# Performance work log

Measured on AMD Instinct MI355X. Metric: run time of the kernel, lower is better.

## Reference

```python
import jax, jax.numpy as jnp
import numpy as np

NUM_HEADS = 16
D_MODEL = 1024
SEQ = 4096
HEAD_DIM = D_MODEL // NUM_HEADS
ROPE_BASE = 10000.0


def _rope(x):
    # x: [h, s, d]  (rotate-half RoPE per head)
    s, d = x.shape[-2], x.shape[-1]
    inv_freq = 1.0 / (ROPE_BASE ** (jnp.arange(0, d, 2, dtype=jnp.float32) / d))  # [d/2]
    ang = jnp.arange(s, dtype=jnp.float32)[:, None] * inv_freq[None, :]           # [s, d/2]
    cos, sin = jnp.cos(ang), jnp.sin(ang)
    x1, x2 = x[..., : d // 2], x[..., d // 2 :]
    return jnp.concatenate([x1 * cos - x2 * sin, x1 * sin + x2 * cos], axis=-1)


def setup_inputs() -> dict:
    key = jax.random.key(0)
    kq, kk, kv, kwq, kwk, kwv = jax.random.split(key, 6)
    scale = 1.0 / np.sqrt(D_MODEL)
    return {
        "q": jax.random.normal(kq, (SEQ, D_MODEL), dtype=jnp.float32),
        "k": jax.random.normal(kk, (SEQ, D_MODEL), dtype=jnp.float32),
        "v": jax.random.normal(kv, (SEQ, D_MODEL), dtype=jnp.float32),
        "mask": jnp.tril(jnp.ones((SEQ, SEQ), dtype=bool)),  # causal
        "Wq": jax.random.normal(kwq, (D_MODEL, D_MODEL), dtype=jnp.float32) * scale,
        "Wk": jax.random.normal(kwk, (D_MODEL, D_MODEL), dtype=jnp.float32) * scale,
        "Wv": jax.random.normal(kwv, (D_MODEL, D_MODEL), dtype=jnp.float32) * scale,
    }


def reference(q, k, v, mask, Wq, Wk, Wv):
    # Projections (eqx Linear: x @ W.T, no bias)
    qp = q @ Wq.T  # [s, d_model]
    kp = k @ Wk.T
    vp = v @ Wv.T
    # split heads: [s, (h d)] -> [h, s, d]
    def split(x):
        return x.reshape(SEQ, NUM_HEADS, HEAD_DIM).transpose(1, 0, 2)
    qh, kh, vh = split(qp), split(kp), split(vp)
    qh = _rope(qh)
    kh = _rope(kh)
    # explicit full logits, masked softmax (matches original, no SDPA)
    logits = jnp.einsum("hqd,hkd->hqk", qh, kh) / jnp.sqrt(jnp.float32(HEAD_DIM))
    logits = jnp.where(mask[None, :, :], logits, -jnp.inf)
    attn = jax.nn.softmax(logits, axis=-1)  # [h, q, k]
    out = jnp.einsum("hqk,hkd->hqd", attn, vh)
    return out.transpose(1, 0, 2).reshape(SEQ, D_MODEL)
```

## Files before the change

### kernel.cpp

```cpp
#include <hip/hip_runtime.h>
#include <math.h>

#define SEQ 4096
#define DMODEL 1024
#define NHEADS 16
#define HDIM 64

typedef __bf16 v8bf __attribute__((ext_vector_type(8)));
typedef float f32x4 __attribute__((ext_vector_type(4)));
typedef float f32x16 __attribute__((ext_vector_type(16)));
typedef int i32x2 __attribute__((ext_vector_type(2)));
typedef int i32x4 __attribute__((ext_vector_type(4)));

#define NPART 4608
#define SCALE_Q 0.18033688011112042f

__device__ __forceinline__ unsigned short f2bf(float f) {
    union { float f; unsigned int u; } v; v.f = f;
    unsigned int u = v.u;
    return (unsigned short)((u + 0x7fffu + ((u >> 16) & 1u)) >> 16);
}

__device__ __forceinline__ int cvtpk(float lo, float hi) {
    int r;
    asm("v_cvt_pk_bf16_f32 %0, %1, %2" : "=v"(r) : "v"(lo), "v"(hi));
    return r;
}

__device__ __forceinline__ void gload16(const unsigned short* g, unsigned short* l) {
    __builtin_amdgcn_global_load_lds(
        (const __attribute__((address_space(1))) unsigned int*)g,
        (__attribute__((address_space(3))) unsigned int*)l, 16, 0, 0);
}

__global__ __launch_bounds__(256) void cast_kernel(
    const float* __restrict__ q, const float* __restrict__ k, const float* __restrict__ v,
    const float* __restrict__ wq, const float* __restrict__ wk, const float* __restrict__ wv,
    unsigned short* __restrict__ xq, unsigned short* __restrict__ xk,
    unsigned short* __restrict__ xv, unsigned short* __restrict__ wb)
{
    const size_t M4 = (size_t)4 << 20, M1 = (size_t)1 << 20;
    size_t i = ((size_t)blockIdx.x * 256 + threadIdx.x) * 8;
    const float* s; unsigned short* d; size_t off;
    if (i < M4)                 { s = q;  d = xq;          off = i; }
    else if (i < 2 * M4)        { s = k;  d = xk;          off = i - M4; }
    else if (i < 3 * M4)        { s = v;  d = xv;          off = i - 2 * M4; }
    else if (i < 3 * M4 + M1)   { s = wq; d = wb;          off = i - 3 * M4; }
    else if (i < 3 * M4 + 2*M1) { s = wk; d = wb + M1;     off = i - 3 * M4 - M1; }
    else                        { s = wv; d = wb + 2 * M1; off = i - 3 * M4 - 2 * M1; }
    float4 a = *reinterpret_cast<const float4*>(s + off);
    float4 b = *reinterpret_cast<const float4*>(s + off + 4);
    uint4 u;
    u.x = (unsigned)cvtpk(a.x, a.y); u.y = (unsigned)cvtpk(a.z, a.w);
    u.z = (unsigned)cvtpk(b.x, b.y); u.w = (unsigned)cvtpk(b.z, b.w);
    *reinterpret_cast<uint4*>(d + off) = u;
}

__global__ __launch_bounds__(256) void proj_rope_kernel(
    const unsigned short* __restrict__ Xq, const unsigned short* __restrict__ Xk,
    const unsigned short* __restrict__ Xv, const unsigned short* __restrict__ Wb,
    unsigned short* __restrict__ qh, unsigned short* __restrict__ kfr,
    unsigned short* __restrict__ vfr)
{
    const int tz = blockIdx.z;
    const unsigned short* __restrict__ X = (tz == 0) ? Xq : (tz == 1) ? Xk : Xv;
    const unsigned short* __restrict__ W = Wb + (size_t)tz * ((size_t)1 << 20);

    const int tid = threadIdx.x;
    const int lane = tid & 63;
    const int wid = tid >> 6;
    const int l15 = lane & 15;
    const int l4 = lane >> 4;
    const int wr = wid >> 1, wc = wid & 1;

    const int m0 = blockIdx.x * 128;
    const int n0 = blockIdx.y * 128;

    __shared__ __align__(16) unsigned short Ab[2][4096];
    __shared__ __align__(16) unsigned short Bb[2][4096];

    int grow[2], gcol[2];
    #pragma unroll
    for (int g = 0; g < 2; ++g) {
        int row = wid * 32 + g * 16 + (lane >> 2);
        grow[g] = row;
        gcol[g] = 8 * ((lane & 3) ^ ((row >> 1) & 3));
    }

    auto STAGE = [&](int b, int kt) {
        const int k0 = kt << 5;
        #pragma unroll
        for (int g = 0; g < 2; ++g) {
            gload16(X + (size_t)(m0 + grow[g]) * DMODEL + k0 + gcol[g],
                    &Ab[b][(wid * 2 + g) * 512]);
            gload16(W + (size_t)(n0 + grow[g]) * DMODEL + k0 + gcol[g],
                    &Bb[b][(wid * 2 + g) * 512]);
        }
    };

    f32x4 acc[4][4] = {};

    STAGE(0, 0);
    for (int kt = 0; kt < 32; ++kt) {
        __syncthreads();
        if (kt < 31) STAGE((kt + 1) & 1, kt + 1);

        const unsigned short* A = Ab[kt & 1];
        const unsigned short* B = Bb[kt & 1];

        v8bf af[4], bfr[4];
        #pragma unroll
        for (int mi = 0; mi < 4; ++mi) {
            int row = wr * 64 + mi * 16 + l15;
            int byte = row * 64 + ((l4 ^ ((row >> 1) & 3)) << 4);
            af[mi] = *reinterpret_cast<const v8bf*>(reinterpret_cast<const char*>(A) + byte);
        }
        #pragma unroll
        for (int ni = 0; ni < 4; ++ni) {
            int row = wc * 64 + ni * 16 + l15;
            int byte = row * 64 + ((l4 ^ ((row >> 1) & 3)) << 4);
            bfr[ni] = *reinterpret_cast<const v8bf*>(reinterpret_cast<const char*>(B) + byte);
        }
        #pragma unroll
        for (int mi = 0; mi < 4; ++mi)
            #pragma unroll
            for (int ni = 0; ni < 4; ++ni)
                acc[mi][ni] = __builtin_amdgcn_mfma_f32_16x16x32_bf16(af[mi], bfr[ni], acc[mi][ni], 0, 0, 0);
    }

    const int h = (n0 >> 6) + wc;
    const int mbase = m0 + wr * 64;
    const int T = blockIdx.x * 2 + wr;

    if (tz == 2) {
        unsigned short* vb = vfr + (size_t)h * 262144 + (size_t)T * 4096;
        #pragma unroll
        for (int mi = 0; mi < 4; ++mi) {
            #pragma unroll
            for (int ni = 0; ni < 4; ++ni) {
                int f = (ni >> 1) * 4 + mi;
                int off = f * 512 + ((l4 >> 1) * 32 + (ni & 1) * 16 + l15) * 8 + (l4 & 1) * 4;
                uint2 pk;
                pk.x = (unsigned)cvtpk(acc[mi][ni][0], acc[mi][ni][1]);
                pk.y = (unsigned)cvtpk(acc[mi][ni][2], acc[mi][ni][3]);
                *reinterpret_cast<uint2*>(vb + off) = pk;
            }
        }
    } else if (tz == 1) {
        unsigned short* kb = kfr + (size_t)h * 262144 + (size_t)T * 4096;
        #pragma unroll
        for (int ni = 0; ni < 2; ++ni) {
            int j = ni * 16 + l15;
            float invf = expf(-(float)j * 0.28782313662425574f);
            #pragma unroll
            for (int mi = 0; mi < 4; ++mi) {
                #pragma unroll
                for (int r = 0; r < 4; ++r) {
                    int m = mbase + mi * 16 + l4 * 4 + r;
                    float ang = (float)m * invf;
                    float sn, cs;
                    sincosf(ang, &sn, &cs);
                    float x1 = acc[mi][ni][r];
                    float x2 = acc[mi][ni + 2][r];
                    int rowoff = ((l15 >> 3) * 32 + (mi & 1) * 16 + l4 * 4 + r) * 8 + (l15 & 7);
                    int fb = (mi >> 1) * 4;
                    kb[(fb + ni) * 512 + rowoff]     = f2bf(x1 * cs - x2 * sn);
                    kb[(fb + ni + 2) * 512 + rowoff] = f2bf(x1 * sn + x2 * cs);
                }
            }
        }
    } else {
        unsigned short* base = qh + (size_t)h * SEQ * HDIM;
        #pragma unroll
        for (int ni = 0; ni < 2; ++ni) {
            int j = ni * 16 + l15;
            float invf = expf(-(float)j * 0.28782313662425574f);
            #pragma unroll
            for (int mi = 0; mi < 4; ++mi) {
                #pragma unroll
                for (int r = 0; r < 4; ++r) {
                    int m = mbase + mi * 16 + l4 * 4 + r;
                    float ang = (float)m * invf;
                    float sn, cs;
                    sincosf(ang, &sn, &cs);
                    sn *= SCALE_Q; cs *= SCALE_Q;
                    float x1 = acc[mi][ni][r];
                    float x2 = acc[mi][ni + 2][r];
                    base[(size_t)m * HDIM + j]      = f2bf(x1 * cs - x2 * sn);
                    base[(size_t)m * HDIM + j + 32] = f2bf(x1 * sn + x2 * cs);
                }
            }
        }
    }
}

__global__ __launch_bounds__(64, 2) void attn_kernel(
    const unsigned short* __restrict__ qh, const unsigned short* __restrict__ kfr,
    const unsigned short* __restrict__ vfr, float* __restrict__ out,
    unsigned short* __restrict__ po, float* __restrict__ ml)
{
    const int lane = threadIdx.x & 63;
    const int l31 = lane & 31;
    const int l5 = lane >> 5;

    const int bid = blockIdx.x;
    const int xcd = bid & 7;
    const int idx = bid >> 3;
    const int hsel = (idx >= 320) ? 1 : 0;
    const int h = (xcd << 1) | hsel;
    const int r = 319 - (idx - hsel * 320);

    int qb, c, nc;
    if (r < 32)       { qb = r;                     c = 0;            nc = 1; }
    else if (r < 96)  { qb = 32 + ((r - 32) >> 1);  c = (r - 32) & 1; nc = 2; }
    else if (r < 192) { int rr = r - 96; qb = 64 + rr / 3; c = rr - (qb - 64) * 3; nc = 3; }
    else              { int rr = r - 192; qb = 96 + (rr >> 2); c = rr & 3; nc = 4; }

    const int q0 = qb * 32;
    const int q = q0 + l31;
    const int nt = (q0 + 32 + 63) >> 6;
    const int t0 = c * 16;
    const int t1 = min(t0 + 16, nt);

    const unsigned short* __restrict__ qbase = qh + ((size_t)h * SEQ + q) * HDIM + l5 * 8;
    const unsigned short* __restrict__ kfh = kfr + (size_t)h * 262144 + lane * 8;
    const unsigned short* __restrict__ vfh = vfr + (size_t)h * 262144 + lane * 8;

    v8bf qf[4];
    #pragma unroll
    for (int dk = 0; dk < 4; ++dk)
        qf[dk] = *reinterpret_cast<const v8bf*>(qbase + dk * 16);

    f32x16 of[2] = {};
    float mreg = -INFINITY, lreg = 0.0f;

    auto LOADK = [&](v8bf (&KB)[8], int T) {
        const unsigned short* kp = kfh + (size_t)T * 4096;
        #pragma unroll
        for (int f = 0; f < 8; ++f)
            KB[f] = *reinterpret_cast<const v8bf*>(kp + f * 512);
    };

    auto ROUND = [&](int T, v8bf (&KC)[8], v8bf (&KN)[8]) {
        v8bf vf[8];
        {
            const unsigned short* vp = vfh + (size_t)T * 4096;
            #pragma unroll
            for (int f = 0; f < 8; ++f)
                vf[f] = *reinterpret_cast<const v8bf*>(vp + f * 512);
        }
        if (T + 1 < t1) LOADK(KN, T + 1);

        f32x16 st[2];
        __builtin_amdgcn_s_setprio(1);
        #pragma unroll
        for (int ns = 0; ns < 2; ++ns) {
            f32x16 acc = {};
            #pragma unroll
            for (int dk = 0; dk < 4; ++dk)
                acc = __builtin_amdgcn_mfma_f32_32x32x16_bf16(KC[ns * 4 + dk], qf[dk], acc, 0, 0, 0);
            st[ns] = acc;
        }
        __builtin_amdgcn_s_setprio(0);

        if (T == nt - 1) {
            const int kvb = T * 64 + 4 * l5;
            #pragma unroll
            for (int ns = 0; ns < 2; ++ns)
                #pragma unroll
                for (int i = 0; i < 16; ++i) {
                    int kv = kvb + ns * 32 + (i & 3) + 8 * (i >> 2);
                    if (kv > q) st[ns][i] = -INFINITY;
                }
        }

        float t16[16];
        #pragma unroll
        for (int i = 0; i < 16; ++i) t16[i] = fmaxf(st[0][i], st[1][i]);
        #pragma unroll
        for (int i = 0; i < 8; ++i) t16[i] = fmaxf(t16[i], t16[i + 8]);
        #pragma unroll
        for (int i = 0; i < 4; ++i) t16[i] = fmaxf(t16[i], t16[i + 4]);
        float pmax = fmaxf(fmaxf(t16[0], t16[1]), fmaxf(t16[2], t16[3]));
        {
            i32x2 sw = __builtin_amdgcn_permlane32_swap(__float_as_int(pmax), __float_as_int(pmax), false, false);
            pmax = fmaxf(__int_as_float(sw.x), __int_as_float(sw.y));
        }

        if (!__all(pmax - mreg <= 8.0f)) {
            float mnew = fmaxf(mreg, pmax);
            float sc = exp2f(mreg - mnew);
            lreg *= sc;
            #pragma unroll
            for (int dt = 0; dt < 2; ++dt)
                #pragma unroll
                for (int i = 0; i < 16; ++i) of[dt][i] *= sc;
            mreg = mnew;
        }

        float ps0 = 0.f, ps1 = 0.f, ps2 = 0.f, ps3 = 0.f;
        #pragma unroll
        for (int ns = 0; ns < 2; ++ns)
            #pragma unroll
            for (int i = 0; i < 16; ++i) {
                float p = exp2f(st[ns][i] - mreg);
                st[ns][i] = p;
                if ((i & 3) == 0) ps0 += p; else if ((i & 3) == 1) ps1 += p;
                else if ((i & 3) == 2) ps2 += p; else ps3 += p;
            }
        lreg += (ps0 + ps1) + (ps2 + ps3);

        v8bf pt[4];
        #pragma unroll
        for (int kb = 0; kb < 4; ++kb) {
            int ns = kb >> 1, kp = (kb & 1) * 8;
            int A0 = cvtpk(st[ns][kp + 0], st[ns][kp + 1]);
            int A1 = cvtpk(st[ns][kp + 2], st[ns][kp + 3]);
            int B0 = cvtpk(st[ns][kp + 4], st[ns][kp + 5]);
            int B1 = cvtpk(st[ns][kp + 6], st[ns][kp + 7]);
            i32x2 s0 = __builtin_amdgcn_permlane32_swap(A0, B0, false, false);
            i32x2 s1 = __builtin_amdgcn_permlane32_swap(A1, B1, false, false);
            i32x4 u; u.x = s0.x; u.y = s1.x; u.z = s0.y; u.w = s1.y;
            v8bf p; __builtin_memcpy(&p, &u, 16);
            pt[kb] = p;
        }

        __builtin_amdgcn_s_setprio(1);
        #pragma unroll
        for (int dt = 0; dt < 2; ++dt)
            #pragma unroll
            for (int kb = 0; kb < 4; ++kb)
                of[dt] = __builtin_amdgcn_mfma_f32_32x32x16_bf16(vf[dt * 4 + kb], pt[kb], of[dt], 0, 0, 0);
        __builtin_amdgcn_s_setprio(0);
    };

    v8bf kA[8], kB[8];
    LOADK(kA, t0);
    int t = t0;
    while (true) {
        ROUND(t, kA, kB);
        if (++t == t1) break;
        ROUND(t, kB, kA);
        if (++t == t1) break;
    }

    {
        i32x2 sw = __builtin_amdgcn_permlane32_swap(__float_as_int(lreg), __float_as_int(lreg), false, false);
        lreg = __int_as_float(sw.x) + __int_as_float(sw.y);
    }

    if (nc == 1) {
        float inv = 1.0f / lreg;
        float* obase = out + (size_t)q * DMODEL + h * HDIM + l5 * 4;
        #pragma unroll
        for (int dt = 0; dt < 2; ++dt)
            #pragma unroll
            for (int g = 0; g < 4; ++g) {
                f32x4 o4;
                o4[0] = of[dt][g * 4 + 0] * inv;
                o4[1] = of[dt][g * 4 + 1] * inv;
                o4[2] = of[dt][g * 4 + 2] * inv;
                o4[3] = of[dt][g * 4 + 3] * inv;
                *reinterpret_cast<f32x4*>(obase + dt * 32 + g * 8) = o4;
            }
    } else {
        const int p = h * 288 + (r - 32);
        unsigned short* pb = po + ((size_t)p * 32 + l31) * 64 + l5 * 4;
        #pragma unroll
        for (int dt = 0; dt < 2; ++dt)
            #pragma unroll
            for (int g = 0; g < 4; ++g) {
                uint2 u;
                u.x = (unsigned)cvtpk(of[dt][g * 4 + 0], of[dt][g * 4 + 1]);
                u.y = (unsigned)cvtpk(of[dt][g * 4 + 2], of[dt][g * 4 + 3]);
                *reinterpret_cast<uint2*>(pb + dt * 32 + g * 8) = u;
            }
        if (l5 == 0) {
            float2 v; v.x = mreg; v.y = lreg;
            reinterpret_cast<float2*>(ml)[(size_t)p * 32 + l31] = v;
        }
    }
}

__global__ __launch_bounds__(256) void combine_kernel(
    const unsigned short* __restrict__ po, const float* __restrict__ ml,
    float* __restrict__ out)
{
    const int b = blockIdx.x;
    const int h = b / 96;
    const int j = b - h * 96;
    const int qb = 32 + j;
    int nc, r0;
    if (qb < 64)      { nc = 2; r0 = 32 + ((qb - 32) << 1); }
    else if (qb < 96) { nc = 3; r0 = 96 + (qb - 64) * 3; }
    else              { nc = 4; r0 = 192 + ((qb - 96) << 2); }
    const int p0 = h * 288 + (r0 - 32);
    const int d = threadIdx.x & 63;
    const int rg = threadIdx.x >> 6;
    const int q0 = qb * 32;

    for (int row = rg; row < 32; row += 4) {
        float mc[4], lc[4];
        float M = -INFINITY;
        #pragma unroll
        for (int ci = 0; ci < 4; ++ci)
            if (ci < nc) {
                float2 v = reinterpret_cast<const float2*>(ml)[(size_t)(p0 + ci) * 32 + row];
                mc[ci] = v.x; lc[ci] = v.y;
                M = fmaxf(M, v.x);
            }
        float L = 0.0f, O = 0.0f;
        #pragma unroll
        for (int ci = 0; ci < 4; ++ci)
            if (ci < nc) {
                float w = exp2f(mc[ci] - M);
                L += lc[ci] * w;
                unsigned int raw = po[((size_t)(p0 + ci) * 32 + row) * 64 + d];
                union { unsigned int u; float f; } cv; cv.u = raw << 16;
                O += cv.f * w;
            }
        out[(size_t)(q0 + row) * DMODEL + h * HDIM + d] = O / L;
    }
}

extern "C" void kernel_launch(void* const* d_in, const int* in_sizes, int n_in,
                              void* d_out, int out_size, void* d_ws, size_t ws_size,
                              hipStream_t stream) {
    (void)in_sizes; (void)n_in; (void)out_size; (void)ws_size;
    const float* q  = (const float*)d_in[0];
    const float* k  = (const float*)d_in[1];
    const float* v  = (const float*)d_in[2];
    const float* Wq = (const float*)d_in[4];
    const float* Wk = (const float*)d_in[5];
    const float* Wv = (const float*)d_in[6];

    const size_t M4 = (size_t)4 << 20;
    unsigned short* qh  = (unsigned short*)d_ws;
    unsigned short* kfr = qh  + M4;
    unsigned short* vfr = kfr + M4;
    unsigned short* scratch = vfr + M4;
    unsigned short* Xbv = scratch;
    unsigned short* Wb  = scratch + M4;
    unsigned short* po  = scratch;
    float* ml = (float*)(po + (size_t)NPART * 32 * 64);
    unsigned short* Xbq = (unsigned short*)d_out;
    unsigned short* Xbk = Xbq + M4;
    float* out = (float*)d_out;

    cast_kernel<<<dim3(7680), 256, 0, stream>>>(q, k, v, Wq, Wk, Wv, Xbq, Xbk, Xbv, Wb);

    dim3 g1(SEQ / 128, DMODEL / 128, 3);
    proj_rope_kernel<<<g1, 256, 0, stream>>>(Xbq, Xbk, Xbv, Wb, qh, kfr, vfr);

    attn_kernel<<<dim3(16 * 320), 64, 0, stream>>>(qh, kfr, vfr, out, po, ml);

    combine_kernel<<<dim3(16 * 96), 256, 0, stream>>>(po, ml, out);
}
```

Baseline: 164.2 us.

## Process two 32-row query blocks per wave to share K/V tile loads

Each attention wave now handles a 64-row query group as two 32-row sub-blocks (A and B), so every K and V tile it loads feeds twice as many MFMAs. This halves K/V global traffic per query and halves the grid size, and the split-chunk indexing and combine kernel are remapped to match. The explicit double-buffered K prefetch is dropped in favour of a simple loop that loads K and V together. Register pressure rises from the doubled Q fragments and accumulators, which may reduce occupancy or expose load latency.

```diff
diff --git a/kernel.cpp b/kernel.cpp
--- a/kernel.cpp
+++ b/kernel.cpp
@@ -206,74 +206,42 @@
     const int bid = blockIdx.x;
     const int xcd = bid & 7;
     const int idx = bid >> 3;
-    const int hsel = (idx >= 320) ? 1 : 0;
+    const int hsel = (idx >= 160) ? 1 : 0;
     const int h = (xcd << 1) | hsel;
-    const int r = 319 - (idx - hsel * 320);
-
-    int qb, c, nc;
-    if (r < 32)       { qb = r;                     c = 0;            nc = 1; }
-    else if (r < 96)  { qb = 32 + ((r - 32) >> 1);  c = (r - 32) & 1; nc = 2; }
-    else if (r < 192) { int rr = r - 96; qb = 64 + rr / 3; c = rr - (qb - 64) * 3; nc = 3; }
-    else              { int rr = r - 192; qb = 96 + (rr >> 2); c = rr & 3; nc = 4; }
-
-    const int q0 = qb * 32;
-    const int q = q0 + l31;
-    const int nt = (q0 + 32 + 63) >> 6;
+    const int r = 159 - (idx - hsel * 160);
+
+    int g, c, nc;
+    if (r < 16)      { g = r;                    c = 0;           nc = 1; }
+    else if (r < 48) { g = 16 + ((r - 16) >> 1); c = (r - 16) & 1; nc = 2; }
+    else if (r < 96) { int rr = r - 48; g = 32 + rr / 3; c = rr - (g - 32) * 3; nc = 3; }
+    else             { int rr = r - 96; g = 48 + (rr >> 2); c = rr & 3; nc = 4; }
+
+    const int q0 = g * 64;
+    const int qA = q0 + l31;
+    const int qB = q0 + 32 + l31;
+    const int nt = g + 1;
     const int t0 = c * 16;
     const int t1 = min(t0 + 16, nt);
 
-    const unsigned short* __restrict__ qbase = qh + ((size_t)h * SEQ + q) * HDIM + l5 * 8;
     const unsigned short* __restrict__ kfh = kfr + (size_t)h * 262144 + lane * 8;
     const unsigned short* __restrict__ vfh = vfr + (size_t)h * 262144 + lane * 8;
 
-    v8bf qf[4];
-    #pragma unroll
-    for (int dk = 0; dk < 4; ++dk)
-        qf[dk] = *reinterpret_cast<const v8bf*>(qbase + dk * 16);
-
-    f32x16 of[2] = {};
-    float mreg = -INFINITY, lreg = 0.0f;
-
-    auto LOADK = [&](v8bf (&KB)[8], int T) {
-        const unsigned short* kp = kfh + (size_t)T * 4096;
-        #pragma unroll
-        for (int f = 0; f < 8; ++f)
-            KB[f] = *reinterpret_cast<const v8bf*>(kp + f * 512);
-    };
-
-    auto ROUND = [&](int T, v8bf (&KC)[8], v8bf (&KN)[8]) {
-        v8bf vf[8];
-        {
-            const unsigned short* vp = vfh + (size_t)T * 4096;
-            #pragma unroll
-            for (int f = 0; f < 8; ++f)
-                vf[f] = *reinterpret_cast<const v8bf*>(vp + f * 512);
-        }
-        if (T + 1 < t1) LOADK(KN, T + 1);
-
-        f32x16 st[2];
-        __builtin_amdgcn_s_setprio(1);
-        #pragma unroll
-        for (int ns = 0; ns < 2; ++ns) {
-            f32x16 acc = {};
-            #pragma unroll
-            for (int dk = 0; dk < 4; ++dk)
-                acc = __builtin_amdgcn_mfma_f32_32x32x16_bf16(KC[ns * 4 + dk], qf[dk], acc, 0, 0, 0);
-            st[ns] = acc;
-        }
-        __builtin_amdgcn_s_setprio(0);
-
-        if (T == nt - 1) {
-            const int kvb = T * 64 + 4 * l5;
-            #pragma unroll
-            for (int ns = 0; ns < 2; ++ns)
-                #pragma unroll
-                for (int i = 0; i < 16; ++i) {
-                    int kv = kvb + ns * 32 + (i & 3) + 8 * (i >> 2);
-                    if (kv > q) st[ns][i] = -INFINITY;
-                }
-        }
-
+    v8bf qfA[4], qfB[4];
+    {
+        const unsigned short* qa = qh + ((size_t)h * SEQ + qA) * HDIM + l5 * 8;
+        const unsigned short* qb = qh + ((size_t)h * SEQ + qB) * HDIM + l5 * 8;
+        #pragma unroll
+        for (int dk = 0; dk < 4; ++dk) {
+            qfA[dk] = *reinterpret_cast<const v8bf*>(qa + dk * 16);
+            qfB[dk] = *reinterpret_cast<const v8bf*>(qb + dk * 16);
+        }
+    }
+
+    f32x16 ofA[2] = {}, ofB[2] = {};
+    float mA = -INFINITY, lA = 0.0f, mB = -INFINITY, lB = 0.0f;
+
+    auto SOFTMAX = [&](f32x16 (&st)[2], f32x16 (&of)[2], float &mreg, float &lreg,
+                       v8bf (&pt)[4]) {
         float t16[16];
         #pragma unroll
         for (int i = 0; i < 16; ++i) t16[i] = fmaxf(st[0][i], st[1][i]);
@@ -286,7 +254,6 @@
             i32x2 sw = __builtin_amdgcn_permlane32_swap(__float_as_int(pmax), __float_as_int(pmax), false, false);
             pmax = fmaxf(__int_as_float(sw.x), __int_as_float(sw.y));
         }
-
         if (!__all(pmax - mreg <= 8.0f)) {
             float mnew = fmaxf(mreg, pmax);
             float sc = exp2f(mreg - mnew);
@@ -297,7 +264,6 @@
                 for (int i = 0; i < 16; ++i) of[dt][i] *= sc;
             mreg = mnew;
         }
-
         float ps0 = 0.f, ps1 = 0.f, ps2 = 0.f, ps3 = 0.f;
         #pragma unroll
         for (int ns = 0; ns < 2; ++ns)
@@ -309,8 +275,6 @@
                 else if ((i & 3) == 2) ps2 += p; else ps3 += p;
             }
         lreg += (ps0 + ps1) + (ps2 + ps3);
-
-        v8bf pt[4];
         #pragma unroll
         for (int kb = 0; kb < 4; ++kb) {
             int ns = kb >> 1, kp = (kb & 1) * 8;
@@ -324,60 +288,120 @@
             v8bf p; __builtin_memcpy(&p, &u, 16);
             pt[kb] = p;
         }
-
+    };
+
+    for (int T = t0; T < t1; ++T) {
+        v8bf kc[8], vf[8];
+        {
+            const unsigned short* kp = kfh + (size_t)T * 4096;
+            #pragma unroll
+            for (int f = 0; f < 8; ++f)
+                kc[f] = *reinterpret_cast<const v8bf*>(kp + f * 512);
+            const unsigned short* vp = vfh + (size_t)T * 4096;
+            #pragma unroll
+            for (int f = 0; f < 8; ++f)
+                vf[f] = *reinterpret_cast<const v8bf*>(vp + f * 512);
+        }
+
+        f32x16 stA[2], stB[2];
         __builtin_amdgcn_s_setprio(1);
         #pragma unroll
+        for (int ns = 0; ns < 2; ++ns) {
+            f32x16 acc = {};
+            #pragma unroll
+            for (int dk = 0; dk < 4; ++dk)
+                acc = __builtin_amdgcn_mfma_f32_32x32x16_bf16(kc[ns * 4 + dk], qfA[dk], acc, 0, 0, 0);
+            stA[ns] = acc;
+        }
+        #pragma unroll
+        for (int ns = 0; ns < 2; ++ns) {
+            f32x16 acc = {};
+            #pragma unroll
+            for (int dk = 0; dk < 4; ++dk)
+                acc = __builtin_amdgcn_mfma_f32_32x32x16_bf16(kc[ns * 4 + dk], qfB[dk], acc, 0, 0, 0);
+            stB[ns] = acc;
+        }
+        __builtin_amdgcn_s_setprio(0);
+
+        if (T == nt - 1) {
+            const int kvb = T * 64 + 4 * l5;
+            #pragma unroll
+            for (int ns = 0; ns < 2; ++ns)
+                #pragma unroll
+                for (int i = 0; i < 16; ++i) {
+                    int kv = kvb + ns * 32 + (i & 3) + 8 * (i >> 2);
+                    if (kv > qA) stA[ns][i] = -INFINITY;
+                    if (kv > qB) stB[ns][i] = -INFINITY;
+                }
+        }
+
+        v8bf ptA[4];
+        SOFTMAX(stA, ofA, mA, lA, ptA);
+        __builtin_amdgcn_s_setprio(1);
+        #pragma unroll
         for (int dt = 0; dt < 2; ++dt)
             #pragma unroll
             for (int kb = 0; kb < 4; ++kb)
-                of[dt] = __builtin_amdgcn_mfma_f32_32x32x16_bf16(vf[dt * 4 + kb], pt[kb], of[dt], 0, 0, 0);
+                ofA[dt] = __builtin_amdgcn_mfma_f32_32x32x16_bf16(vf[dt * 4 + kb], ptA[kb], ofA[dt], 0, 0, 0);
         __builtin_amdgcn_s_setprio(0);
-    };
-
-    v8bf kA[8], kB[8];
-    LOADK(kA, t0);
-    int t = t0;
-    while (true) {
-        ROUND(t, kA, kB);
-        if (++t == t1) break;
-        ROUND(t, kB, kA);
-        if (++t == t1) break;
+
+        v8bf ptB[4];
+        SOFTMAX(stB, ofB, mB, lB, ptB);
+        __builtin_amdgcn_s_setprio(1);
+        #pragma unroll
+        for (int dt = 0; dt < 2; ++dt)
+            #pragma unroll
+            for (int kb = 0; kb < 4; ++kb)
+                ofB[dt] = __builtin_amdgcn_mfma_f32_32x32x16_bf16(vf[dt * 4 + kb], ptB[kb], ofB[dt], 0, 0, 0);
+        __builtin_amdgcn_s_setprio(0);
     }
 
     {
-        i32x2 sw = __builtin_amdgcn_permlane32_swap(__float_as_int(lreg), __float_as_int(lreg), false, false);
-        lreg = __int_as_float(sw.x) + __int_as_float(sw.y);
+        i32x2 swA = __builtin_amdgcn_permlane32_swap(__float_as_int(lA), __float_as_int(lA), false, false);
+        lA = __int_as_float(swA.x) + __int_as_float(swA.y);
+        i32x2 swB = __builtin_amdgcn_permlane32_swap(__float_as_int(lB), __float_as_int(lB), false, false);
+        lB = __int_as_float(swB.x) + __int_as_float(swB.y);
     }
 
     if (nc == 1) {
-        float inv = 1.0f / lreg;
-        float* obase = out + (size_t)q * DMODEL + h * HDIM + l5 * 4;
+        float invA = 1.0f / lA, invB = 1.0f / lB;
+        float* oa = out + (size_t)qA * DMODEL + h * HDIM + l5 * 4;
+        float* ob = out + (size_t)qB * DMODEL + h * HDIM + l5 * 4;
         #pragma unroll
         for (int dt = 0; dt < 2; ++dt)
             #pragma unroll
-            for (int g = 0; g < 4; ++g) {
+            for (int gg = 0; gg < 4; ++gg) {
                 f32x4 o4;
-                o4[0] = of[dt][g * 4 + 0] * inv;
-                o4[1] = of[dt][g * 4 + 1] * inv;
-                o4[2] = of[dt][g * 4 + 2] * inv;
-                o4[3] = of[dt][g * 4 + 3] * inv;
-                *reinterpret_cast<f32x4*>(obase + dt * 32 + g * 8) = o4;
+                o4[0] = ofA[dt][gg * 4 + 0] * invA; o4[1] = ofA[dt][gg * 4 + 1] * invA;
+                o4[2] = ofA[dt][gg * 4 + 2] * invA; o4[3] = ofA[dt][gg * 4 + 3] * invA;
+                *reinterpret_cast<f32x4*>(oa + dt * 32 + gg * 8) = o4;
+                o4[0] = ofB[dt][gg * 4 + 0] * invB; o4[1] = ofB[dt][gg * 4 + 1] * invB;
+                o4[2] = ofB[dt][gg * 4 + 2] * invB; o4[3] = ofB[dt][gg * 4 + 3] * invB;
+                *reinterpret_cast<f32x4*>(ob + dt * 32 + gg * 8) = o4;
             }
     } else {
-        const int p = h * 288 + (r - 32);
-        unsigned short* pb = po + ((size_t)p * 32 + l31) * 64 + l5 * 4;
+        const int mc = r - 16;
+        const int pA = h * 288 + mc * 2;
+        const int pB = pA + 1;
+        unsigned short* pa = po + ((size_t)pA * 32 + l31) * 64 + l5 * 4;
+        unsigned short* pb = po + ((size_t)pB * 32 + l31) * 64 + l5 * 4;
         #pragma unroll
         for (int dt = 0; dt < 2; ++dt)
             #pragma unroll
-            for (int g = 0; g < 4; ++g) {
+            for (int gg = 0; gg < 4; ++gg) {
                 uint2 u;
-                u.x = (unsigned)cvtpk(of[dt][g * 4 + 0], of[dt][g * 4 + 1]);
-                u.y = (unsigned)cvtpk(of[dt][g * 4 + 2], of[dt][g * 4 + 3]);
-                *reinterpret_cast<uint2*>(pb + dt * 32 + g * 8) = u;
+                u.x = (unsigned)cvtpk(ofA[dt][gg * 4 + 0], ofA[dt][gg * 4 + 1]);
+                u.y = (unsigned)cvtpk(ofA[dt][gg * 4 + 2], ofA[dt][gg * 4 + 3]);
+                *reinterpret_cast<uint2*>(pa + dt * 32 + gg * 8) = u;
+                u.x = (unsigned)cvtpk(ofB[dt][gg * 4 + 0], ofB[dt][gg * 4 + 1]);
+                u.y = (unsigned)cvtpk(ofB[dt][gg * 4 + 2], ofB[dt][gg * 4 + 3]);
+                *reinterpret_cast<uint2*>(pb + dt * 32 + gg * 8) = u;
             }
         if (l5 == 0) {
-            float2 v; v.x = mreg; v.y = lreg;
-            reinterpret_cast<float2*>(ml)[(size_t)p * 32 + l31] = v;
+            float2 va; va.x = mA; va.y = lA;
+            reinterpret_cast<float2*>(ml)[(size_t)pA * 32 + l31] = va;
+            float2 vb; vb.x = mB; vb.y = lB;
+            reinterpret_cast<float2*>(ml)[(size_t)pB * 32 + l31] = vb;
         }
     }
 }
@@ -389,15 +413,16 @@
     const int b = blockIdx.x;
     const int h = b / 96;
     const int j = b - h * 96;
-    const int qb = 32 + j;
-    int nc, r0;
-    if (qb < 64)      { nc = 2; r0 = 32 + ((qb - 32) << 1); }
-    else if (qb < 96) { nc = 3; r0 = 96 + (qb - 64) * 3; }
-    else              { nc = 4; r0 = 192 + ((qb - 96) << 2); }
-    const int p0 = h * 288 + (r0 - 32);
+    const int gm = 16 + (j >> 1);
+    const int sub = j & 1;
+    int nc, mcs;
+    if (gm < 32)      { nc = 2; mcs = (gm - 16) * 2; }
+    else if (gm < 48) { nc = 3; mcs = 32 + (gm - 32) * 3; }
+    else              { nc = 4; mcs = 80 + (gm - 48) * 4; }
+    const int pbase = h * 288 + mcs * 2 + sub;
     const int d = threadIdx.x & 63;
     const int rg = threadIdx.x >> 6;
-    const int q0 = qb * 32;
+    const int q0 = gm * 64 + sub * 32;
 
     for (int row = rg; row < 32; row += 4) {
         float mc[4], lc[4];
@@ -405,7 +430,7 @@
         #pragma unroll
         for (int ci = 0; ci < 4; ++ci)
             if (ci < nc) {
-                float2 v = reinterpret_cast<const float2*>(ml)[(size_t)(p0 + ci) * 32 + row];
+                float2 v = reinterpret_cast<const float2*>(ml)[(size_t)(pbase + ci * 2) * 32 + row];
                 mc[ci] = v.x; lc[ci] = v.y;
                 M = fmaxf(M, v.x);
             }
@@ -415,7 +440,7 @@
             if (ci < nc) {
                 float w = exp2f(mc[ci] - M);
                 L += lc[ci] * w;
-                unsigned int raw = po[((size_t)(p0 + ci) * 32 + row) * 64 + d];
+                unsigned int raw = po[((size_t)(pbase + ci * 2) * 32 + row) * 64 + d];
                 union { unsigned int u; float f; } cv; cv.u = raw << 16;
                 O += cv.f * w;
             }
@@ -452,7 +477,7 @@
     dim3 g1(SEQ / 128, DMODEL / 128, 3);
     proj_rope_kernel<<<g1, 256, 0, stream>>>(Xbq, Xbk, Xbv, Wb, qh, kfr, vfr);
 
-    attn_kernel<<<dim3(16 * 320), 64, 0, stream>>>(qh, kfr, vfr, out, po, ml);
+    attn_kernel<<<dim3(2560), 64, 0, stream>>>(qh, kfr, vfr, out, po, ml);
 
     combine_kernel<<<dim3(16 * 96), 256, 0, stream>>>(po, ml, out);
 }
```

Measured after the change: 181.4 us. 1.11x slower.
